# Performance work log

Measured on AMD Instinct MI355X. Metric: run time of the kernel, lower is better.

The kernel has to match this reference:

```python
import jax, jax.numpy as jnp
import numpy as np

B, T, DIM, HEADS = 8, 1024, 256, 8
DH = DIM // HEADS


def setup_inputs() -> dict:
    key = jax.random.key(0)
    ks = jax.random.split(key, 8)
    x = jax.random.normal(ks[0], (B, T, DIM), dtype=jnp.float32)
    adj = jax.random.randint(ks[1], (B, 1, T, T), 0, 2).astype(jnp.int32)
    label = jax.random.randint(ks[2], (B,), 0, 10).astype(jnp.int64)
    Wq = jax.random.normal(ks[3], (DH, DH), dtype=jnp.float32) * 0.05
    Wk = jax.random.normal(ks[4], (DH, DH), dtype=jnp.float32) * 0.05
    Wv = jax.random.normal(ks[5], (DH, DH), dtype=jnp.float32) * 0.05
    Lam = jax.random.normal(ks[6], (HEADS, HEADS), dtype=jnp.float32)
    Wproj = jax.random.normal(ks[7], (DIM, DIM), dtype=jnp.float32) * 0.05
    return dict(x=x, adj=adj, label=label, Wq=Wq, Wk=Wk, Wv=Wv, Lam=Lam, Wproj=Wproj)


def reference(x, adj, label, Wq, Wk, Wv, Lam, Wproj):
    b, t, dim = x.shape
    h, dh = HEADS, dim // HEADS
    scale = dim ** (-0.5)  # note: scale uses full dim, as in the source
    # b t (h d) -> b h t d
    xh = x.reshape(b, t, h, dh).transpose(0, 2, 1, 3)
    adj_f = adj.astype(x.dtype)  # [b,1,t,t], broadcasts over heads

    def gcn(W, A):
        # graph conv: A @ (x @ W), per-head, weight shared across heads
        return jnp.matmul(A, jnp.einsum('bhtd,de->bhte', xh, W))

    q = gcn(Wq, adj_f)  # [b,h,t,dh]
    k = gcn(Wk, adj_f)
    attn = jnp.einsum('bhld,bhtd->bhlt', q, k) * scale
    attn = jax.nn.leaky_relu(attn, negative_slope=0.01)
    # cross-head Lambda mixing: new_head_i = sum_j Lam[i,j] * attn_head_j
    attn = jnp.einsum('ij,bjlt->bilt', Lam, attn)
    # layer_index=0 < depth//4=3 -> adjacency masking is active
    attn = jnp.where(adj > 0, attn, -jnp.inf)
    attn = jax.nn.softmax(attn, axis=-1)  # rep_adj [b,h,t,t]
    v = jnp.matmul(attn, jnp.einsum('bhtd,de->bhte', xh, Wv))  # GCN with attn as adjacency
    v = v.transpose(0, 2, 1, 3).reshape(b, t, dim)  # b h t d -> b t (h d)
    v = jax.nn.gelu(v, approximate=False)
    out = v @ Wproj.T  # nn.Linear, no bias
    return out, attn
```

## Files before the change

kernel.cpp:

```cpp
#include <hip/hip_runtime.h>
#include <cmath>

#define TT 1024
#define BB 8

typedef __attribute__((ext_vector_type(4))) float f4;
typedef __attribute__((ext_vector_type(4))) unsigned int u4;
typedef __attribute__((ext_vector_type(8))) short s8v;

__device__ __forceinline__ ushort f2bf(float x) {
  unsigned u = __builtin_bit_cast(unsigned, x);
  unsigned r = (u + 0x7FFFu + ((u >> 16) & 1u)) >> 16;
  return (ushort)r;
}
__device__ __forceinline__ float bf2f(ushort b) {
  unsigned u = ((unsigned)b) << 16;
  return __builtin_bit_cast(float, u);
}
__device__ __forceinline__ void st8(ushort* p, const ushort* v) {
  u4 w;
  w.x = (unsigned)v[0] | ((unsigned)v[1] << 16);
  w.y = (unsigned)v[2] | ((unsigned)v[3] << 16);
  w.z = (unsigned)v[4] | ((unsigned)v[5] << 16);
  w.w = (unsigned)v[6] | ((unsigned)v[7] << 16);
  *(u4*)p = w;
}

__global__ __launch_bounds__(256, 2) void k_xw(
    const float* __restrict__ x, const float* __restrict__ Wq,
    const float* __restrict__ Wk, const float* __restrict__ Wv,
    ushort* __restrict__ xTqhi, ushort* __restrict__ xTqlo,
    ushort* __restrict__ xTkhi, ushort* __restrict__ xTklo,
    ushort* __restrict__ vT) {
  __shared__ float xs[16][256];
  int bid = blockIdx.x;
  int b = bid & 7, t0 = (bid >> 3) * 16;
  int tid = threadIdx.x;
#pragma unroll
  for (int i = 0; i < 4; ++i) {
    int e = i * 256 + tid;
    int t = e >> 6, c4 = (e & 63) * 4;
    *(f4*)&xs[t][c4] = *(const f4*)&x[((size_t)(b * 1024 + t0 + t)) * 256 + c4];
  }
  int c = tid, h = c >> 5, d = c & 31;
  float wqr[32], wkr[32], wvr[32];
#pragma unroll
  for (int e = 0; e < 32; ++e) {
    wqr[e] = Wq[e * 32 + d] * 0.0625f;
    wkr[e] = Wk[e * 32 + d];
    wvr[e] = Wv[e * 32 + d];
  }
  __syncthreads();
  size_t rowq = ((size_t)(b * 256 + c)) * 1024 + t0;
#pragma unroll
  for (int tg = 0; tg < 2; ++tg) {
    ushort qh[8], ql[8], kh[8], kl[8], vh[8];
#pragma unroll
    for (int tt = 0; tt < 8; ++tt) {
      int t = tg * 8 + tt;
      float aq = 0.f, ak = 0.f, av = 0.f;
#pragma unroll
      for (int e = 0; e < 32; ++e) {
        float xe = xs[t][h * 32 + e];
        aq = fmaf(xe, wqr[e], aq);
        ak = fmaf(xe, wkr[e], ak);
        av = fmaf(xe, wvr[e], av);
      }
      ushort hq = f2bf(aq); qh[tt] = hq; ql[tt] = f2bf(aq - bf2f(hq));
      ushort hk = f2bf(ak); kh[tt] = hk; kl[tt] = f2bf(ak - bf2f(hk));
      vh[tt] = f2bf(av);
    }
    st8(xTqhi + rowq + tg * 8, qh);
    st8(xTqlo + rowq + tg * 8, ql);
    st8(xTkhi + rowq + tg * 8, kh);
    st8(xTklo + rowq + tg * 8, kl);
    st8(vT    + rowq + tg * 8, vh);
  }
}

__global__ __launch_bounds__(256, 2) void k_gcn(
    const int* __restrict__ adj,
    const ushort* __restrict__ xTqhi, const ushort* __restrict__ xTqlo,
    const ushort* __restrict__ xTkhi, const ushort* __restrict__ xTklo,
    ushort* __restrict__ qhi, ushort* __restrict__ qlo,
    ushort* __restrict__ khi, ushort* __restrict__ klo) {
  int bid = blockIdx.x;
  int ct = bid & 3, lt = ((bid >> 2) & 15) * 64, b = bid >> 6;
  int nt = ct >> 1, cbase = (ct & 1) * 128;
  const ushort* XH = (nt ? xTkhi : xTqhi) + (size_t)b * 256 * 1024;
  const ushort* XL = (nt ? xTklo : xTqlo) + (size_t)b * 256 * 1024;
  ushort* OH = (nt ? khi : qhi) + (size_t)b * 1024 * 256;
  ushort* OL = (nt ? klo : qlo) + (size_t)b * 1024 * 256;
  const int* AD = adj + (size_t)b * 1024 * 1024;
  int tid = threadIdx.x, wid = tid >> 6, lane = tid & 63;
  int lrow = lane & 15, lk = lane >> 4;
  int wr = wid >> 1, wc = wid & 1;
  int rbase = lt + wr * 32;
  int cb2 = cbase + wc * 64;
  f4 acc[2][4];
#pragma unroll
  for (int i = 0; i < 2; ++i)
#pragma unroll
    for (int j = 0; j < 4; ++j) acc[i][j] = (f4)(0.f);

  for (int k0 = 0; k0 < 1024; k0 += 32) {
    s8v afr[2];
#pragma unroll
    for (int rq = 0; rq < 2; ++rq) {
      const int* ap = &AD[(size_t)(rbase + rq * 16 + lrow) * 1024 + k0 + lk * 8];
      int4 a0 = *(const int4*)ap;
      int4 a1 = *(const int4*)(ap + 4);
      u4 fw;
      fw.x = (a0.x ? 0x3F80u : 0u) | (a0.y ? 0x3F800000u : 0u);
      fw.y = (a0.z ? 0x3F80u : 0u) | (a0.w ? 0x3F800000u : 0u);
      fw.z = (a1.x ? 0x3F80u : 0u) | (a1.y ? 0x3F800000u : 0u);
      fw.w = (a1.z ? 0x3F80u : 0u) | (a1.w ? 0x3F800000u : 0u);
      afr[rq] = __builtin_bit_cast(s8v, fw);
    }
#pragma unroll
    for (int nq = 0; nq < 4; ++nq) {
      int col = cb2 + nq * 16 + lrow;
      s8v bh = *(const s8v*)&XH[(size_t)col * 1024 + k0 + lk * 8];
      s8v bl = *(const s8v*)&XL[(size_t)col * 1024 + k0 + lk * 8];
#pragma unroll
      for (int rq = 0; rq < 2; ++rq) {
        acc[rq][nq] = __builtin_amdgcn_mfma_f32_16x16x32_bf16(afr[rq], bh, acc[rq][nq], 0, 0, 0);
        acc[rq][nq] = __builtin_amdgcn_mfma_f32_16x16x32_bf16(afr[rq], bl, acc[rq][nq], 0, 0, 0);
      }
    }
  }
#pragma unroll
  for (int rq = 0; rq < 2; ++rq)
#pragma unroll
    for (int nq = 0; nq < 4; ++nq)
#pragma unroll
      for (int e = 0; e < 4; ++e) {
        float v = acc[rq][nq][e];
        int row = rbase + rq * 16 + lk * 4 + e;
        int col = cb2 + nq * 16 + lrow;
        ushort hi = f2bf(v);
        ushort lo = f2bf(v - bf2f(hi));
        OH[(size_t)row * 256 + col] = hi;
        OL[(size_t)row * 256 + col] = lo;
      }
}

__global__ __launch_bounds__(256, 2) void k_stats(
    const ushort* __restrict__ qhi, const ushort* __restrict__ qlo,
    const ushort* __restrict__ khi, const ushort* __restrict__ klo,
    const int* __restrict__ adj, const float* __restrict__ Lam,
    float* __restrict__ pm, float* __restrict__ ps) {
  __shared__ float sm_m[2][32][8];
  __shared__ float sm_s[2][32][8];
  int bid = blockIdx.x;
  int b = bid >> 8;
  int lt = ((bid >> 3) & 31) << 5;
  int tc = bid & 7;
  int tid = threadIdx.x, wid = tid >> 6, lane = tid & 63;
  int lrow = lane & 15, lk = lane >> 4;
  int wr = wid >> 1, wc = wid & 1;
  const ushort* QH = qhi + (size_t)b * 1024 * 256;
  const ushort* QL = qlo + (size_t)b * 1024 * 256;
  const ushort* KH = khi + (size_t)b * 1024 * 256;
  const ushort* KL = klo + (size_t)b * 1024 * 256;
  const int* AD = adj + (size_t)b * 1024 * 1024;

  s8v qfh[8], qfl[8];
  int qrow = lt + wr * 16 + lrow;
#pragma unroll
  for (int h = 0; h < 8; ++h) {
    qfh[h] = *(const s8v*)&QH[(size_t)qrow * 256 + h * 32 + lk * 8];
    qfl[h] = *(const s8v*)&QL[(size_t)qrow * 256 + h * 32 + lk * 8];
  }
  float ms[4][8], ss[4][8];
#pragma unroll
  for (int e = 0; e < 4; ++e)
#pragma unroll
    for (int i2 = 0; i2 < 8; ++i2) { ms[e][i2] = -3.0e38f; ss[e][i2] = 0.f; }

  for (int it = 0; it < 4; ++it) {
    int t0 = tc * 128 + (it * 2 + wc) * 16;
    f4 acc[8];
#pragma unroll
    for (int h = 0; h < 8; ++h) {
      s8v kh = *(const s8v*)&KH[(size_t)(t0 + lrow) * 256 + h * 32 + lk * 8];
      s8v kl = *(const s8v*)&KL[(size_t)(t0 + lrow) * 256 + h * 32 + lk * 8];
      f4 a = (f4)(0.f);
      a = __builtin_amdgcn_mfma_f32_16x16x32_bf16(qfh[h], kh, a, 0, 0, 0);
      a = __builtin_amdgcn_mfma_f32_16x16x32_bf16(qfh[h], kl, a, 0, 0, 0);
      a = __builtin_amdgcn_mfma_f32_16x16x32_bf16(qfl[h], kh, a, 0, 0, 0);
      acc[h] = a;
    }
#pragma unroll
    for (int e = 0; e < 4; ++e) {
      int row = lt + wr * 16 + lk * 4 + e;
      int a = AD[(size_t)row * 1024 + t0 + lrow];
      bool pred = a > 0;
      float raw[8];
#pragma unroll
      for (int h = 0; h < 8; ++h) { float v = acc[h][e]; raw[h] = fmaxf(v, 0.01f * v); }
#pragma unroll
      for (int i2 = 0; i2 < 8; ++i2) {
        float s = 0.f;
#pragma unroll
        for (int j = 0; j < 8; ++j) s = fmaf(Lam[i2 * 8 + j], raw[j], s);
        float d = s - ms[e][i2];
        float ex = __expf(fminf(d, -d));
        float snew = (d > 0.f) ? fmaf(ss[e][i2], ex, 1.f) : (ss[e][i2] + ex);
        float mnew = fmaxf(ms[e][i2], s);
        if (pred) { ss[e][i2] = snew; ms[e][i2] = mnew; }
      }
    }
  }
#pragma unroll
  for (int e = 0; e < 4; ++e)
#pragma unroll
    for (int i2 = 0; i2 < 8; ++i2) {
      float mm = ms[e][i2], sv = ss[e][i2];
      for (int off = 1; off < 16; off <<= 1) {
        float om = __shfl_xor(mm, off, 64);
        float os = __shfl_xor(sv, off, 64);
        float d = mm - om;
        float ex = __expf(fminf(d, -d));
        float sA = fmaf(os, ex, sv);
        float sB = fmaf(sv, ex, os);
        sv = (d >= 0.f) ? sA : sB;
        mm = fmaxf(mm, om);
      }
      ms[e][i2] = mm; ss[e][i2] = sv;
    }
  if (lrow == 0) {
#pragma unroll
    for (int e = 0; e < 4; ++e)
#pragma unroll
      for (int i2 = 0; i2 < 8; ++i2) {
        sm_m[wc][wr * 16 + lk * 4 + e][i2] = ms[e][i2];
        sm_s[wc][wr * 16 + lk * 4 + e][i2] = ss[e][i2];
      }
  }
  __syncthreads();
  {
    int rw = tid >> 3, i2 = tid & 7;
    float m0 = sm_m[0][rw][i2], m1 = sm_m[1][rw][i2];
    float s0 = sm_s[0][rw][i2], s1 = sm_s[1][rw][i2];
    float M = fmaxf(m0, m1);
    float S = s0 * __expf(m0 - M) + s1 * __expf(m1 - M);
    size_t R = ((size_t)(b * 8 + i2) * 1024 + lt + rw);
    pm[R * 8 + tc] = M;
    ps[R * 8 + tc] = S;
  }
}

__global__ __launch_bounds__(256) void k_reduce(
    const float* __restrict__ pm, const float* __restrict__ ps,
    float* __restrict__ fm, float* __restrict__ fr) {
  int R = blockIdx.x * 256 + threadIdx.x;
  f4 m0 = *(const f4*)&pm[(size_t)R * 8];
  f4 m1 = *(const f4*)&pm[(size_t)R * 8 + 4];
  f4 s0 = *(const f4*)&ps[(size_t)R * 8];
  f4 s1 = *(const f4*)&ps[(size_t)R * 8 + 4];
  float M = fmaxf(fmaxf(fmaxf(m0.x, m0.y), fmaxf(m0.z, m0.w)),
                  fmaxf(fmaxf(m1.x, m1.y), fmaxf(m1.z, m1.w)));
  float S = s0.x * __expf(m0.x - M) + s0.y * __expf(m0.y - M) +
            s0.z * __expf(m0.z - M) + s0.w * __expf(m0.w - M) +
            s1.x * __expf(m1.x - M) + s1.y * __expf(m1.y - M) +
            s1.z * __expf(m1.z - M) + s1.w * __expf(m1.w - M);
  fm[R] = M;
  fr[R] = 1.f / S;
}

__global__ __launch_bounds__(256, 2) void k_final(
    const ushort* __restrict__ qhi, const ushort* __restrict__ qlo,
    const ushort* __restrict__ khi, const ushort* __restrict__ klo,
    const int* __restrict__ adj, const float* __restrict__ Lam,
    const float* __restrict__ fm, const float* __restrict__ fr,
    float* __restrict__ attn) {
  __shared__ float fin_m[32][8];
  __shared__ float fin_r[32][8];
  int bid = blockIdx.x;
  int b = bid >> 8;
  int lt = ((bid >> 3) & 31) << 5;
  int tc = bid & 7;
  int tid = threadIdx.x, wid = tid >> 6, lane = tid & 63;
  int lrow = lane & 15, lk = lane >> 4;
  int wr = wid >> 1, wc = wid & 1;
  const ushort* QH = qhi + (size_t)b * 1024 * 256;
  const ushort* QL = qlo + (size_t)b * 1024 * 256;
  const ushort* KH = khi + (size_t)b * 1024 * 256;
  const ushort* KL = klo + (size_t)b * 1024 * 256;
  const int* AD = adj + (size_t)b * 1024 * 1024;
  float* AT = attn + (size_t)b * 8 * 1024 * 1024;
  {
    int rw = tid >> 3, i2 = tid & 7;
    size_t R = ((size_t)(b * 8 + i2) * 1024 + lt + rw);
    fin_m[rw][i2] = fm[R];
    fin_r[rw][i2] = fr[R];
  }
  s8v qfh[8], qfl[8];
  int qrow = lt + wr * 16 + lrow;
#pragma unroll
  for (int h = 0; h < 8; ++h) {
    qfh[h] = *(const s8v*)&QH[(size_t)qrow * 256 + h * 32 + lk * 8];
    qfl[h] = *(const s8v*)&QL[(size_t)qrow * 256 + h * 32 + lk * 8];
  }
  __syncthreads();
  float ms[4][8], rs[4][8];
#pragma unroll
  for (int e = 0; e < 4; ++e)
#pragma unroll
    for (int i2 = 0; i2 < 8; ++i2) {
      ms[e][i2] = fin_m[wr * 16 + lk * 4 + e][i2];
      rs[e][i2] = fin_r[wr * 16 + lk * 4 + e][i2];
    }
  for (int it = 0; it < 4; ++it) {
    int t0 = tc * 128 + (it * 2 + wc) * 16;
    f4 acc[8];
#pragma unroll
    for (int h = 0; h < 8; ++h) {
      s8v kh = *(const s8v*)&KH[(size_t)(t0 + lrow) * 256 + h * 32 + lk * 8];
      s8v kl = *(const s8v*)&KL[(size_t)(t0 + lrow) * 256 + h * 32 + lk * 8];
      f4 a = (f4)(0.f);
      a = __builtin_amdgcn_mfma_f32_16x16x32_bf16(qfh[h], kh, a, 0, 0, 0);
      a = __builtin_amdgcn_mfma_f32_16x16x32_bf16(qfh[h], kl, a, 0, 0, 0);
      a = __builtin_amdgcn_mfma_f32_16x16x32_bf16(qfl[h], kh, a, 0, 0, 0);
      acc[h] = a;
    }
#pragma unroll
    for (int e = 0; e < 4; ++e) {
      int row = lt + wr * 16 + lk * 4 + e;
      int a = AD[(size_t)row * 1024 + t0 + lrow];
      bool pred = a > 0;
      float raw[8];
#pragma unroll
      for (int h = 0; h < 8; ++h) { float v = acc[h][e]; raw[h] = fmaxf(v, 0.01f * v); }
#pragma unroll
      for (int i2 = 0; i2 < 8; ++i2) {
        float s = 0.f;
#pragma unroll
        for (int j = 0; j < 8; ++j) s = fmaf(Lam[i2 * 8 + j], raw[j], s);
        float p = pred ? __expf(s - ms[e][i2]) * rs[e][i2] : 0.f;
        AT[((size_t)i2 * 1024 + row) * 1024 + t0 + lrow] = p;
      }
    }
  }
}

__global__ __launch_bounds__(256, 4) void k_pv(
    const float* __restrict__ attn, const ushort* __restrict__ vT,
    float* __restrict__ g) {
  __shared__ ushort Vs[32][136];
  __shared__ unsigned pt[64 * 128 / 2];
  int bid = blockIdx.x;
  int b = bid & 7, h = (bid >> 3) & 7, lt = (bid >> 6) * 64;
  int tid = threadIdx.x, wid = tid >> 6, lane = tid & 63;
  int lrow = lane & 15, lk = lane >> 4;
  const float* AT = attn + ((size_t)(b * 8 + h) * 1024 + lt) * 1024;
  const ushort* VTb = vT + (size_t)(b * 256 + h * 32) * 1024;
  char* ptb = (char*)pt;
  f4 acc[2];
  acc[0] = (f4)(0.f); acc[1] = (f4)(0.f);

  for (int tc = 0; tc < 1024; tc += 128) {
    {
      int col = tid >> 3, toff = (tid & 7) * 16;
      u4 v0 = *(const u4*)&VTb[(size_t)col * 1024 + tc + toff];
      u4 v1 = *(const u4*)&VTb[(size_t)col * 1024 + tc + toff + 8];
      *(u4*)&Vs[col][toff] = v0;
      *(u4*)&Vs[col][toff + 8] = v1;
    }
    {
      int row = tid >> 2, tq = (tid & 3) * 32;
      const float* src = &AT[(size_t)row * 1024 + tc + tq];
#pragma unroll
      for (int i = 0; i < 4; ++i) {
        f4 p0 = *(const f4*)&src[i * 8];
        f4 p1 = *(const f4*)&src[i * 8 + 4];
        u4 pk;
        pk.x = (unsigned)f2bf(p0[0]) | ((unsigned)f2bf(p0[1]) << 16);
        pk.y = (unsigned)f2bf(p0[2]) | ((unsigned)f2bf(p0[3]) << 16);
        pk.z = (unsigned)f2bf(p1[0]) | ((unsigned)f2bf(p1[1]) << 16);
        pk.w = (unsigned)f2bf(p1[2]) | ((unsigned)f2bf(p1[3]) << 16);
        int t = tq + i * 8;
        int boff = row * 256 + ((t * 2) ^ ((row & 7) << 4));
        *(u4*)(ptb + boff) = pk;
      }
    }
    __syncthreads();
    int prow = wid * 16 + lrow;
#pragma unroll
    for (int ks = 0; ks < 4; ++ks) {
      int t = ks * 32 + lk * 8;
      int aoff = prow * 256 + ((t * 2) ^ ((prow & 7) << 4));
      s8v af = *(const s8v*)(ptb + aoff);
#pragma unroll
      for (int nq = 0; nq < 2; ++nq) {
        s8v bf = *(const s8v*)&Vs[nq * 16 + lrow][t];
        acc[nq] = __builtin_amdgcn_mfma_f32_16x16x32_bf16(af, bf, acc[nq], 0, 0, 0);
      }
    }
    __syncthreads();
  }
#pragma unroll
  for (int nq = 0; nq < 2; ++nq)
#pragma unroll
    for (int e = 0; e < 4; ++e) {
      float v = acc[nq][e];
      float ge = 0.5f * v * (1.f + erff(v * 0.70710678118654752f));
      int row = lt + wid * 16 + lk * 4 + e;
      int col = h * 32 + nq * 16 + lrow;
      g[(size_t)(b * 1024 + row) * 256 + col] = ge;
    }
}

__global__ __launch_bounds__(256, 2) void k_proj(
    const float* __restrict__ g, const float* __restrict__ Wp,
    float* __restrict__ out) {
  __shared__ float g_s[16][68];
  __shared__ float w_s[16][68];
  int rt = blockIdx.y * 64;
  int it = blockIdx.x * 64;
  int tid = threadIdx.x;
  int tx = tid & 15, ty = tid >> 4;
  int r4 = tid >> 2, cq = tid & 3;
  float acc[4][4] = {};
  for (int kc = 0; kc < 256; kc += 16) {
    float4 gv = *(const float4*)&g[(size_t)(rt + r4) * 256 + kc + cq * 4];
    g_s[cq * 4 + 0][r4] = gv.x; g_s[cq * 4 + 1][r4] = gv.y;
    g_s[cq * 4 + 2][r4] = gv.z; g_s[cq * 4 + 3][r4] = gv.w;
    float4 wv = *(const float4*)&Wp[(size_t)(it + r4) * 256 + kc + cq * 4];
    w_s[cq * 4 + 0][r4] = wv.x; w_s[cq * 4 + 1][r4] = wv.y;
    w_s[cq * 4 + 2][r4] = wv.z; w_s[cq * 4 + 3][r4] = wv.w;
    __syncthreads();
#pragma unroll
    for (int k = 0; k < 16; ++k) {
      float4 a = *(const float4*)&g_s[k][ty * 4];
      float4 bb = *(const float4*)&w_s[k][tx * 4];
      acc[0][0] = fmaf(a.x, bb.x, acc[0][0]); acc[0][1] = fmaf(a.x, bb.y, acc[0][1]);
      acc[0][2] = fmaf(a.x, bb.z, acc[0][2]); acc[0][3] = fmaf(a.x, bb.w, acc[0][3]);
      acc[1][0] = fmaf(a.y, bb.x, acc[1][0]); acc[1][1] = fmaf(a.y, bb.y, acc[1][1]);
      acc[1][2] = fmaf(a.y, bb.z, acc[1][2]); acc[1][3] = fmaf(a.y, bb.w, acc[1][3]);
      acc[2][0] = fmaf(a.z, bb.x, acc[2][0]); acc[2][1] = fmaf(a.z, bb.y, acc[2][1]);
      acc[2][2] = fmaf(a.z, bb.z, acc[2][2]); acc[2][3] = fmaf(a.z, bb.w, acc[2][3]);
      acc[3][0] = fmaf(a.w, bb.x, acc[3][0]); acc[3][1] = fmaf(a.w, bb.y, acc[3][1]);
      acc[3][2] = fmaf(a.w, bb.z, acc[3][2]); acc[3][3] = fmaf(a.w, bb.w, acc[3][3]);
    }
    __syncthreads();
  }
#pragma unroll
  for (int i = 0; i < 4; ++i) {
    float4 o = make_float4(acc[i][0], acc[i][1], acc[i][2], acc[i][3]);
    *(float4*)&out[(size_t)(rt + ty * 4 + i) * 256 + it + tx * 4] = o;
  }
}

extern "C" void kernel_launch(void* const* d_in, const int* in_sizes, int n_in,
                              void* d_out, int out_size, void* d_ws, size_t ws_size,
                              hipStream_t stream) {
  const float* x   = (const float*)d_in[0];
  const int*   adj = (const int*)d_in[1];
  const float* Wq  = (const float*)d_in[3];
  const float* Wk  = (const float*)d_in[4];
  const float* Wv  = (const float*)d_in[5];
  const float* Lam = (const float*)d_in[6];
  const float* Wp  = (const float*)d_in[7];

  float* out  = (float*)d_out;
  float* attn = out + (size_t)BB * TT * 256;

  const size_t SZ = (size_t)8 * 1024 * 256;
  char* base = (char*)d_ws;
  ushort* xTqhi = (ushort*)(base + 0 * SZ * 2);
  ushort* xTqlo = (ushort*)(base + 1 * SZ * 2);
  ushort* xTkhi = (ushort*)(base + 2 * SZ * 2);
  ushort* xTklo = (ushort*)(base + 3 * SZ * 2);
  ushort* vT    = (ushort*)(base + 4 * SZ * 2);
  ushort* qhi   = (ushort*)(base + 5 * SZ * 2);
  ushort* qlo   = (ushort*)(base + 6 * SZ * 2);
  ushort* khi   = (ushort*)(base + 7 * SZ * 2);
  ushort* klo   = (ushort*)(base + 8 * SZ * 2);
  float*  gbuf  = (float*)(base + 9 * SZ * 2);
  float*  pm    = (float*)(base + 9 * SZ * 2 + SZ * 4);
  float*  ps    = pm + 524288;
  float*  fmb   = ps + 524288;
  float*  frb   = fmb + 65536;

  k_xw<<<512, 256, 0, stream>>>(x, Wq, Wk, Wv, xTqhi, xTqlo, xTkhi, xTklo, vT);
  k_gcn<<<512, 256, 0, stream>>>(adj, xTqhi, xTqlo, xTkhi, xTklo, qhi, qlo, khi, klo);
  k_stats<<<2048, 256, 0, stream>>>(qhi, qlo, khi, klo, adj, Lam, pm, ps);
  k_reduce<<<256, 256, 0, stream>>>(pm, ps, fmb, frb);
  k_final<<<2048, 256, 0, stream>>>(qhi, qlo, khi, klo, adj, Lam, fmb, frb, attn);
  k_pv<<<1024, 256, 0, stream>>>(attn, vT, gbuf);
  k_proj<<<dim3(4, 128), 256, 0, stream>>>(gbuf, Wp, out);
}
```

Before: 454.6 us.

## Store raw masked logits in stats pass and normalize inside PV kernel

The stats kernel now writes the Lambda-mixed logits (or -1e30 where adj is masked) straight into the attention buffer. The separate final kernel, which recomputed QK^T, Lambda mixing and read adj a second time, is removed. The PV kernel reads those logits, applies exp(s-m)*r, writes the normalized probabilities back in place, and uses them for the PV MMA. The aim is to drop the second QK recompute and adj read, in exchange for an extra full read-modify-write pass over the large attention tensor.

```diff
diff --git a/kernel.cpp b/kernel.cpp
--- a/kernel.cpp
+++ b/kernel.cpp
@@ -145,11 +145,11 @@
       }
 }
 
-__global__ __launch_bounds__(256, 2) void k_stats(
+__global__ __launch_bounds__(256, 2) void k_stats_w(
     const ushort* __restrict__ qhi, const ushort* __restrict__ qlo,
     const ushort* __restrict__ khi, const ushort* __restrict__ klo,
     const int* __restrict__ adj, const float* __restrict__ Lam,
-    float* __restrict__ pm, float* __restrict__ ps) {
+    float* __restrict__ sout, float* __restrict__ pm, float* __restrict__ ps) {
   __shared__ float sm_m[2][32][8];
   __shared__ float sm_s[2][32][8];
   int bid = blockIdx.x;
@@ -164,6 +164,7 @@
   const ushort* KH = khi + (size_t)b * 1024 * 256;
   const ushort* KL = klo + (size_t)b * 1024 * 256;
   const int* AD = adj + (size_t)b * 1024 * 1024;
+  float* AT = sout + (size_t)b * 8 * 1024 * 1024;
 
   s8v qfh[8], qfl[8];
   int qrow = lt + wr * 16 + lrow;
@@ -204,6 +205,7 @@
         float s = 0.f;
 #pragma unroll
         for (int j = 0; j < 8; ++j) s = fmaf(Lam[i2 * 8 + j], raw[j], s);
+        AT[((size_t)i2 * 1024 + row) * 1024 + t0 + lrow] = pred ? s : -1.0e30f;
         float d = s - ms[e][i2];
         float ex = __expf(fminf(d, -d));
         float snew = (d > 0.f) ? fmaf(ss[e][i2], ex, 1.f) : (ss[e][i2] + ex);
@@ -269,84 +271,9 @@
   fr[R] = 1.f / S;
 }
 
-__global__ __launch_bounds__(256, 2) void k_final(
-    const ushort* __restrict__ qhi, const ushort* __restrict__ qlo,
-    const ushort* __restrict__ khi, const ushort* __restrict__ klo,
-    const int* __restrict__ adj, const float* __restrict__ Lam,
+__global__ __launch_bounds__(256, 4) void k_pv_fin(
+    float* __restrict__ attn, const ushort* __restrict__ vT,
     const float* __restrict__ fm, const float* __restrict__ fr,
-    float* __restrict__ attn) {
-  __shared__ float fin_m[32][8];
-  __shared__ float fin_r[32][8];
-  int bid = blockIdx.x;
-  int b = bid >> 8;
-  int lt = ((bid >> 3) & 31) << 5;
-  int tc = bid & 7;
-  int tid = threadIdx.x, wid = tid >> 6, lane = tid & 63;
-  int lrow = lane & 15, lk = lane >> 4;
-  int wr = wid >> 1, wc = wid & 1;
-  const ushort* QH = qhi + (size_t)b * 1024 * 256;
-  const ushort* QL = qlo + (size_t)b * 1024 * 256;
-  const ushort* KH = khi + (size_t)b * 1024 * 256;
-  const ushort* KL = klo + (size_t)b * 1024 * 256;
-  const int* AD = adj + (size_t)b * 1024 * 1024;
-  float* AT = attn + (size_t)b * 8 * 1024 * 1024;
-  {
-    int rw = tid >> 3, i2 = tid & 7;
-    size_t R = ((size_t)(b * 8 + i2) * 1024 + lt + rw);
-    fin_m[rw][i2] = fm[R];
-    fin_r[rw][i2] = fr[R];
-  }
-  s8v qfh[8], qfl[8];
-  int qrow = lt + wr * 16 + lrow;
-#pragma unroll
-  for (int h = 0; h < 8; ++h) {
-    qfh[h] = *(const s8v*)&QH[(size_t)qrow * 256 + h * 32 + lk * 8];
-    qfl[h] = *(const s8v*)&QL[(size_t)qrow * 256 + h * 32 + lk * 8];
-  }
-  __syncthreads();
-  float ms[4][8], rs[4][8];
-#pragma unroll
-  for (int e = 0; e < 4; ++e)
-#pragma unroll
-    for (int i2 = 0; i2 < 8; ++i2) {
-      ms[e][i2] = fin_m[wr * 16 + lk * 4 + e][i2];
-      rs[e][i2] = fin_r[wr * 16 + lk * 4 + e][i2];
-    }
-  for (int it = 0; it < 4; ++it) {
-    int t0 = tc * 128 + (it * 2 + wc) * 16;
-    f4 acc[8];
-#pragma unroll
-    for (int h = 0; h < 8; ++h) {
-      s8v kh = *(const s8v*)&KH[(size_t)(t0 + lrow) * 256 + h * 32 + lk * 8];
-      s8v kl = *(const s8v*)&KL[(size_t)(t0 + lrow) * 256 + h * 32 + lk * 8];
-      f4 a = (f4)(0.f);
-      a = __builtin_amdgcn_mfma_f32_16x16x32_bf16(qfh[h], kh, a, 0, 0, 0);
-      a = __builtin_amdgcn_mfma_f32_16x16x32_bf16(qfh[h], kl, a, 0, 0, 0);
-      a = __builtin_amdgcn_mfma_f32_16x16x32_bf16(qfl[h], kh, a, 0, 0, 0);
-      acc[h] = a;
-    }
-#pragma unroll
-    for (int e = 0; e < 4; ++e) {
-      int row = lt + wr * 16 + lk * 4 + e;
-      int a = AD[(size_t)row * 1024 + t0 + lrow];
-      bool pred = a > 0;
-      float raw[8];
-#pragma unroll
-      for (int h = 0; h < 8; ++h) { float v = acc[h][e]; raw[h] = fmaxf(v, 0.01f * v); }
-#pragma unroll
-      for (int i2 = 0; i2 < 8; ++i2) {
-        float s = 0.f;
-#pragma unroll
-        for (int j = 0; j < 8; ++j) s = fmaf(Lam[i2 * 8 + j], raw[j], s);
-        float p = pred ? __expf(s - ms[e][i2]) * rs[e][i2] : 0.f;
-        AT[((size_t)i2 * 1024 + row) * 1024 + t0 + lrow] = p;
-      }
-    }
-  }
-}
-
-__global__ __launch_bounds__(256, 4) void k_pv(
-    const float* __restrict__ attn, const ushort* __restrict__ vT,
     float* __restrict__ g) {
   __shared__ ushort Vs[32][136];
   __shared__ unsigned pt[64 * 128 / 2];
@@ -354,9 +281,13 @@
   int b = bid & 7, h = (bid >> 3) & 7, lt = (bid >> 6) * 64;
   int tid = threadIdx.x, wid = tid >> 6, lane = tid & 63;
   int lrow = lane & 15, lk = lane >> 4;
-  const float* AT = attn + ((size_t)(b * 8 + h) * 1024 + lt) * 1024;
+  float* AT = attn + ((size_t)(b * 8 + h) * 1024 + lt) * 1024;
   const ushort* VTb = vT + (size_t)(b * 256 + h * 32) * 1024;
   char* ptb = (char*)pt;
+  int srow = tid >> 2, tq = (tid & 3) * 32;
+  size_t ridx0 = (size_t)(b * 8 + h) * 1024 + lt;
+  float mm = fm[ridx0 + srow];
+  float rr = fr[ridx0 + srow];
   f4 acc[2];
   acc[0] = (f4)(0.f); acc[1] = (f4)(0.f);
 
@@ -369,19 +300,25 @@
       *(u4*)&Vs[col][toff + 8] = v1;
     }
     {
-      int row = tid >> 2, tq = (tid & 3) * 32;
-      const float* src = &AT[(size_t)row * 1024 + tc + tq];
+      float* src = &AT[(size_t)srow * 1024 + tc + tq];
 #pragma unroll
       for (int i = 0; i < 4; ++i) {
         f4 p0 = *(const f4*)&src[i * 8];
         f4 p1 = *(const f4*)&src[i * 8 + 4];
+#pragma unroll
+        for (int q = 0; q < 4; ++q) {
+          p0[q] = __expf(p0[q] - mm) * rr;
+          p1[q] = __expf(p1[q] - mm) * rr;
+        }
+        *(f4*)&src[i * 8] = p0;
+        *(f4*)&src[i * 8 + 4] = p1;
         u4 pk;
         pk.x = (unsigned)f2bf(p0[0]) | ((unsigned)f2bf(p0[1]) << 16);
         pk.y = (unsigned)f2bf(p0[2]) | ((unsigned)f2bf(p0[3]) << 16);
         pk.z = (unsigned)f2bf(p1[0]) | ((unsigned)f2bf(p1[1]) << 16);
         pk.w = (unsigned)f2bf(p1[2]) | ((unsigned)f2bf(p1[3]) << 16);
         int t = tq + i * 8;
-        int boff = row * 256 + ((t * 2) ^ ((row & 7) << 4));
+        int boff = srow * 256 + ((t * 2) ^ ((srow & 7) << 4));
         *(u4*)(ptb + boff) = pk;
       }
     }
@@ -486,9 +423,8 @@
 
   k_xw<<<512, 256, 0, stream>>>(x, Wq, Wk, Wv, xTqhi, xTqlo, xTkhi, xTklo, vT);
   k_gcn<<<512, 256, 0, stream>>>(adj, xTqhi, xTqlo, xTkhi, xTklo, qhi, qlo, khi, klo);
-  k_stats<<<2048, 256, 0, stream>>>(qhi, qlo, khi, klo, adj, Lam, pm, ps);
+  k_stats_w<<<2048, 256, 0, stream>>>(qhi, qlo, khi, klo, adj, Lam, attn, pm, ps);
   k_reduce<<<256, 256, 0, stream>>>(pm, ps, fmb, frb);
-  k_final<<<2048, 256, 0, stream>>>(qhi, qlo, khi, klo, adj, Lam, fmb, frb, attn);
-  k_pv<<<1024, 256, 0, stream>>>(attn, vT, gbuf);
+  k_pv_fin<<<1024, 256, 0, stream>>>(attn, vT, fmb, frb, gbuf);
   k_proj<<<dim3(4, 128), 256, 0, stream>>>(gbuf, Wp, out);
 }
```

Result: faster. 425.3 us (median of 2 runs) (-6.4%).
